# Performance work log

Hardware: AMD Instinct MI355X
Metric: run time of the kernel (lower is better)

## Reference

```python
import jax, jax.numpy as jnp
import numpy as np

B, S, E, KD = 4, 2048, 1024, 1024

def setup_inputs() -> dict:
    key = jax.random.key(0)
    k1, k2, k3, k4 = jax.random.split(key, 4)
    # nn.Linear weights are [out_features, in_features]
    x = jax.random.normal(k1, (B, S, E), dtype=jnp.float32)
    W_q = jax.random.normal(k2, (KD, E), dtype=jnp.float32) * (E ** -0.5)
    W_k = jax.random.normal(k3, (KD, E), dtype=jnp.float32) * (E ** -0.5)
    W_v = jax.random.normal(k4, (E, E), dtype=jnp.float32) * (E ** -0.5)
    return {"x": x, "W_q": W_q, "W_k": W_k, "W_v": W_v}

def reference(x, W_q, W_k, W_v):
    # Projections: y = x @ W.T  (torch Linear convention)
    Q = jnp.einsum('bse,ke->bsk', x, W_q)   # [B,S,KD]
    K = jnp.einsum('bse,ke->bsk', x, W_k)   # [B,S,KD]
    V = jnp.einsum('bse,fe->bsf', x, W_v)   # [B,S,E]
    key_dim = W_q.shape[0]
    scores = jnp.einsum('bqk,bsk->bqs', Q, K) / jnp.sqrt(jnp.asarray(key_dim, x.dtype))
    S_len = x.shape[1]
    causal = jnp.tril(jnp.ones((S_len, S_len), dtype=bool))  # [S,S]
    scores = jnp.where(causal, scores, -jnp.inf)
    weights = jax.nn.softmax(scores, axis=-1)                # [B,S,S]
    out = jnp.einsum('bqs,bsf->bqf', weights, V)             # [B,S,E]
    return out
```

## Files before the change

### kernel.cpp

```cpp
#include <hip/hip_runtime.h>

typedef _Float16 f16;
typedef _Float16 f16x8 __attribute__((ext_vector_type(8)));
typedef float    f32x4 __attribute__((ext_vector_type(4)));

__device__ __forceinline__ void gld_lds16(const void* g, void* l) {
    __builtin_amdgcn_global_load_lds((__attribute__((address_space(1))) void*)g,
                                     (__attribute__((address_space(3))) void*)l,
                                     16, 0, 0);
}

#define BARRIER() do { asm volatile("" ::: "memory"); \
                       __builtin_amdgcn_s_barrier();  \
                       asm volatile("" ::: "memory"); } while (0)

template<bool SB, bool SA, int VM>
__device__ __forceinline__ void tile256(
    f32x4 (&acc)[8][4],
    const f16* Ak0, const f16* Ak1, const f16* Bk0, const f16* Bk1,
    const f16* gBn, f16* lBn,
    const f16* gAn, f16* lAn,
    int lda, int ldb)
{
    f16x8 a0[8], a1[8], b0[4], b1[4];
    #pragma unroll
    for (int mf = 0; mf < 8; mf++) a0[mf] = *(const f16x8*)(Ak0 + mf * 1024);
    #pragma unroll
    for (int nf = 0; nf < 4; nf++) b0[nf] = *(const f16x8*)(Bk0 + nf * 1024);
    if (SB) {
        gld_lds16(gBn,                  lBn);
        gld_lds16(gBn + (long)64 * ldb, lBn + 4096);
    }
    BARRIER();
    __builtin_amdgcn_s_setprio(1);
    #pragma unroll
    for (int mf = 0; mf < 4; mf++)
        #pragma unroll
        for (int nf = 0; nf < 4; nf++)
            acc[mf][nf] = __builtin_amdgcn_mfma_f32_16x16x32_f16(
                a0[mf], b0[nf], acc[mf][nf], 0, 0, 0);
    __builtin_amdgcn_s_setprio(0);
    BARRIER();
    #pragma unroll
    for (int mf = 0; mf < 8; mf++) a1[mf] = *(const f16x8*)(Ak1 + mf * 1024);
    #pragma unroll
    for (int nf = 0; nf < 4; nf++) b1[nf] = *(const f16x8*)(Bk1 + nf * 1024);
    if (SB) {
        gld_lds16(gBn + (long)128 * ldb, lBn + 8192);
        gld_lds16(gBn + (long)192 * ldb, lBn + 12288);
    }
    BARRIER();
    __builtin_amdgcn_s_setprio(1);
    #pragma unroll
    for (int mf = 4; mf < 8; mf++)
        #pragma unroll
        for (int nf = 0; nf < 4; nf++)
            acc[mf][nf] = __builtin_amdgcn_mfma_f32_16x16x32_f16(
                a0[mf], b0[nf], acc[mf][nf], 0, 0, 0);
    __builtin_amdgcn_s_setprio(0);
    asm volatile("s_waitcnt lgkmcnt(0)" ::: "memory");
    BARRIER();
    if (SA) {
        gld_lds16(gAn,                  lAn);
        gld_lds16(gAn + (long)64 * lda, lAn + 4096);
    }
    BARRIER();
    __builtin_amdgcn_s_setprio(1);
    #pragma unroll
    for (int mf = 0; mf < 4; mf++)
        #pragma unroll
        for (int nf = 0; nf < 4; nf++)
            acc[mf][nf] = __builtin_amdgcn_mfma_f32_16x16x32_f16(
                a1[mf], b1[nf], acc[mf][nf], 0, 0, 0);
    __builtin_amdgcn_s_setprio(0);
    BARRIER();
    if (SA) {
        gld_lds16(gAn + (long)128 * lda, lAn + 8192);
        gld_lds16(gAn + (long)192 * lda, lAn + 12288);
    }
    BARRIER();
    __builtin_amdgcn_s_setprio(1);
    #pragma unroll
    for (int mf = 4; mf < 8; mf++)
        #pragma unroll
        for (int nf = 0; nf < 4; nf++)
            acc[mf][nf] = __builtin_amdgcn_mfma_f32_16x16x32_f16(
                a1[mf], b1[nf], acc[mf][nf], 0, 0, 0);
    __builtin_amdgcn_s_setprio(0);
    if (VM == 4)      asm volatile("s_waitcnt vmcnt(4)" ::: "memory");
    else if (VM == 0) asm volatile("s_waitcnt vmcnt(0)" ::: "memory");
    BARRIER();
}

__global__ void __launch_bounds__(512, 2)
gemm256_k1024(const f16* __restrict__ A, const f16* __restrict__ B,
              f16* __restrict__ C, int lda, int ldb, int ldc)
{
    const int i0 = blockIdx.y * 256;
    const int j0 = blockIdx.x * 256;

    __shared__ f16 L[2 * 32768] __attribute__((aligned(16)));

    const int tid  = threadIdx.x;
    const int lane = tid & 63;
    const int wave = tid >> 6;
    const int wm = wave >> 2, wn = wave & 3;
    const int row16 = lane & 15, quad = lane >> 4;
    const int swz = row16 & 7;

    const int c0 = (quad ^ swz) * 8;
    const int c1 = ((quad + 4) ^ swz) * 8;
    const f16* A0k0 = L + (wm * 128 + row16) * 64 + c0;
    const f16* A0k1 = L + (wm * 128 + row16) * 64 + c1;
    const f16* B0k0 = L + 16384 + (wn * 64 + row16) * 64 + c0;
    const f16* B0k1 = L + 16384 + (wn * 64 + row16) * 64 + c1;

    const int srow = tid >> 3;
    const int scol = ((tid & 7) ^ (srow & 7)) * 8;
    const f16* gA = A + (long)(i0 + srow) * lda + scol;
    const f16* gB = B + (long)(j0 + srow) * ldb + scol;
    f16* lA0 = L + tid * 8;
    f16* lB0 = L + 16384 + tid * 8;
    f16* lA1 = L + 32768 + tid * 8;
    f16* lB1 = L + 32768 + 16384 + tid * 8;

    gld_lds16(gA,                   lA0);
    gld_lds16(gA + (long)64 * lda,  lA0 + 4096);
    gld_lds16(gA + (long)128 * lda, lA0 + 8192);
    gld_lds16(gA + (long)192 * lda, lA0 + 12288);
    gld_lds16(gB,                   lB0);
    gld_lds16(gB + (long)64 * ldb,  lB0 + 4096);
    gld_lds16(gB + (long)128 * ldb, lB0 + 8192);
    gld_lds16(gB + (long)192 * ldb, lB0 + 12288);
    gld_lds16(gA + 64,                   lA1);
    gld_lds16(gA + 64 + (long)64 * lda,  lA1 + 4096);
    gld_lds16(gA + 64 + (long)128 * lda, lA1 + 8192);
    gld_lds16(gA + 64 + (long)192 * lda, lA1 + 12288);

    f32x4 acc[8][4] = {};

    asm volatile("s_waitcnt vmcnt(4)" ::: "memory");
    BARRIER();

    for (int t = 0; t < 14; t += 2) {
        tile256<true, true, 4>(acc, A0k0, A0k1, B0k0, B0k1,
                               gB + (t + 1) * 64, lB1,
                               gA + (t + 2) * 64, lA0, lda, ldb);
        tile256<true, true, 4>(acc, A0k0 + 32768, A0k1 + 32768,
                               B0k0 + 32768, B0k1 + 32768,
                               gB + (t + 2) * 64, lB0,
                               gA + (t + 3) * 64, lA1, lda, ldb);
    }
    tile256<true, false, 0>(acc, A0k0, A0k1, B0k0, B0k1,
                            gB + 15 * 64, lB1, nullptr, nullptr, lda, ldb);
    tile256<false, false, -1>(acc, A0k0 + 32768, A0k1 + 32768,
                              B0k0 + 32768, B0k1 + 32768,
                              nullptr, nullptr, nullptr, nullptr, lda, ldb);

    #pragma unroll
    for (int mf = 0; mf < 8; mf++) {
        const int r0 = i0 + wm * 128 + mf * 16 + quad * 4;
        #pragma unroll
        for (int nf = 0; nf < 4; nf++) {
            const int c = j0 + wn * 64 + nf * 16 + row16;
            #pragma unroll
            for (int r = 0; r < 4; r++)
                C[(long)(r0 + r) * ldc + c] = (f16)acc[mf][nf][r];
        }
    }
}

template<typename OutT, int MODE>
__global__ void __launch_bounds__(256)
gemm_bt(const f16* __restrict__ A, const f16* __restrict__ B, OutT* __restrict__ C,
        int lda, int ldb, int ldc, int K, float scale,
        long sA, long sB, long sC)
{
    const int bz = blockIdx.z;
    A += (long)bz * sA;
    B += (long)bz * sB;
    C += (long)bz * sC;

    int bx = blockIdx.x, by = blockIdx.y;
    if (MODE == 1) {
        const int t = bx;
        int y = 0;
        while ((y + 1) * (y + 2) <= t) y++;
        by = y;
        bx = t - y * (y + 1);
    }
    if (MODE == 2 && (blockIdx.z & 2)) by = (int)gridDim.y - 1 - by;

    const int i0 = by * 128;
    const int j0 = bx * 64;
    int Keff = K;
    if (MODE == 2) Keff = min(K, i0 + 128);

    __shared__ f16 As[128 * 64] __attribute__((aligned(16)));
    __shared__ f16 Bs[64 * 64]  __attribute__((aligned(16)));

    const int tid  = threadIdx.x;
    const int lane = tid & 63;
    const int wave = tid >> 6;
    const int row16 = lane & 15;
    const int quad  = lane >> 4;
    const int swz   = row16 & 7;
    const int wr = (wave >> 1) * 64;
    const int wc = (wave & 1) * 32;

    const int srow = tid >> 3;
    const int scol = ((tid & 7) ^ (srow & 7)) * 8;
    const f16* gA = A + (long)(i0 + srow) * lda + scol;
    const f16* gB = B + (long)(j0 + srow) * ldb + scol;
    f16* lA = As + tid * 8;
    f16* lB = Bs + tid * 8;

    f32x4 acc[4][2] = {};

    for (int k0 = 0; k0 < Keff; k0 += 64) {
        gld_lds16(gA + k0,                  lA);
        gld_lds16(gA + k0 + (long)32 * lda, lA + 32 * 64);
        gld_lds16(gA + k0 + (long)64 * lda, lA + 64 * 64);
        gld_lds16(gA + k0 + (long)96 * lda, lA + 96 * 64);
        gld_lds16(gB + k0,                  lB);
        gld_lds16(gB + k0 + (long)32 * ldb, lB + 32 * 64);
        __syncthreads();

        #pragma unroll
        for (int kk = 0; kk < 2; kk++) {
            f16x8 af[4], bf[2];
            #pragma unroll
            for (int t = 0; t < 4; t++)
                af[t] = *(const f16x8*)(As + (wr + t * 16 + row16) * 64
                                           + (((kk * 4 + quad) ^ swz) * 8));
            #pragma unroll
            for (int t = 0; t < 2; t++)
                bf[t] = *(const f16x8*)(Bs + (wc + t * 16 + row16) * 64
                                           + (((kk * 4 + quad) ^ swz) * 8));
            #pragma unroll
            for (int mt = 0; mt < 4; mt++)
                #pragma unroll
                for (int nt = 0; nt < 2; nt++)
                    acc[mt][nt] = __builtin_amdgcn_mfma_f32_16x16x32_f16(
                        af[mt], bf[nt], acc[mt][nt], 0, 0, 0);
        }
        __syncthreads();
    }

    #pragma unroll
    for (int mt = 0; mt < 4; mt++) {
        const int r0 = i0 + wr + mt * 16 + quad * 4;
        #pragma unroll
        for (int nt = 0; nt < 2; nt++) {
            const int c = j0 + wc + nt * 16 + row16;
            #pragma unroll
            for (int r = 0; r < 4; r++)
                C[(long)(r0 + r) * ldc + c] = (OutT)(acc[mt][nt][r] * scale);
        }
    }
}

__global__ void __launch_bounds__(256)
softmax_causal(f16* __restrict__ Sc)
{
    const int S = 2048;
    const long rowg = blockIdx.x;
    const long b = rowg >> 11;
    const int  i = (int)(rowg & 2047);
    f16* row = Sc + ((b * S + i) * (long)S);
    const int L = ((i >> 7) + 1) << 7;

    const int tid = threadIdx.x;
    const int c0  = tid * 8;
    const int lane = tid & 63, wave = tid >> 6;
    const bool act = c0 < L;

    float v[8];
    float m = -3.4e38f;
    if (act) {
        f16x8 in = *(const f16x8*)(row + c0);
        #pragma unroll
        for (int j = 0; j < 8; j++) {
            const bool ok = (c0 + j) <= i;
            v[j] = ok ? (float)in[j] : -3.4e38f;
            m = fmaxf(m, v[j]);
        }
    }
    #pragma unroll
    for (int off = 32; off > 0; off >>= 1)
        m = fmaxf(m, __shfl_down(m, off, 64));
    __shared__ float redm[4];
    if (lane == 0) redm[wave] = m;
    __syncthreads();
    const float m0 = fmaxf(fmaxf(redm[0], redm[1]), fmaxf(redm[2], redm[3]));

    float e[8];
    float s = 0.f;
    if (act) {
        #pragma unroll
        for (int j = 0; j < 8; j++) {
            const bool ok = (c0 + j) <= i;
            e[j] = ok ? __expf(v[j] - m0) : 0.f;
            s += e[j];
        }
    }
    #pragma unroll
    for (int off = 32; off > 0; off >>= 1)
        s += __shfl_down(s, off, 64);
    __shared__ float reds[4];
    if (lane == 0) reds[wave] = s;
    __syncthreads();
    const float inv = 1.f / (reds[0] + reds[1] + reds[2] + reds[3]);

    if (act) {
        f16x8 o;
        #pragma unroll
        for (int j = 0; j < 8; j++) o[j] = (f16)(e[j] * inv);
        *(f16x8*)(row + c0) = o;
    }
}

__global__ void __launch_bounds__(256)
convert_all(const float* __restrict__ x, const float* __restrict__ Wq,
            const float* __restrict__ Wk, const float* __restrict__ Wv,
            f16* __restrict__ xh, f16* __restrict__ wh)
{
    const long blk = blockIdx.x;
    const float* src;
    f16* dst;
    long base;
    if (blk < 4096)      { src = x;  dst = xh;                    base = blk * 2048; }
    else if (blk < 4608) { src = Wq; dst = wh;                    base = (blk - 4096) * 2048; }
    else if (blk < 5120) { src = Wk; dst = wh + 1024L * 1024;     base = (blk - 4608) * 2048; }
    else                 { src = Wv; dst = wh + 2L * 1024 * 1024; base = (blk - 5120) * 2048; }
    const long i = base + (long)threadIdx.x * 8;
    f32x4 a = *(const f32x4*)(src + i);
    f32x4 b = *(const f32x4*)(src + i + 4);
    f16x8 o;
    o[0] = (f16)a[0]; o[1] = (f16)a[1]; o[2] = (f16)a[2]; o[3] = (f16)a[3];
    o[4] = (f16)b[0]; o[5] = (f16)b[1]; o[6] = (f16)b[2]; o[7] = (f16)b[3];
    *(f16x8*)(dst + i) = o;
}

extern "C" void kernel_launch(void* const* d_in, const int* in_sizes, int n_in,
                              void* d_out, int out_size, void* d_ws, size_t ws_size,
                              hipStream_t stream)
{
    (void)in_sizes; (void)n_in; (void)out_size; (void)ws_size;
    const float* x  = (const float*)d_in[0];
    const float* Wq = (const float*)d_in[1];
    const float* Wk = (const float*)d_in[2];
    const float* Wv = (const float*)d_in[3];
    float* out = (float*)d_out;

    const long NX = 4L * 2048 * 1024;
    const long NW = 1024L * 1024;

    char* p = (char*)d_ws;
    f16* xh  = (f16*)p; p += NX * 2;
    f16* wh  = (f16*)p; p += 3 * NW * 2;
    f16* QKh = (f16*)p; p += 2 * NX * 2;
    f16* Vt  = (f16*)p; p += NX * 2;
    f16* Sc  = (f16*)p; p += 4L * 2048 * 2048 * 2;
    f16* wvh = wh + 2L * NW;

    convert_all<<<5632, 256, 0, stream>>>(x, Wq, Wk, Wv, xh, wh);

    gemm256_k1024<<<dim3(8, 32, 1), 512, 0, stream>>>(
        xh, wh, QKh, 1024, 1024, 2048);
    gemm_bt<f16, 0><<<dim3(128, 8, 1), 256, 0, stream>>>(
        wvh, xh, Vt, 1024, 1024, 8192, 1024, 1.f, 0, 0, 0);

    gemm_bt<f16, 1><<<dim3(272, 1, 4), 256, 0, stream>>>(
        QKh, QKh + 1024, Sc, 2048, 2048, 2048, 1024, 0.03125f,
        2048L * 2048, 2048L * 2048, 2048L * 2048);

    softmax_causal<<<4 * 2048, 256, 0, stream>>>(Sc);

    gemm_bt<float, 2><<<dim3(16, 16, 4), 256, 0, stream>>>(
        Sc, Vt, out, 2048, 8192, 1024, 2048, 1.f,
        2048L * 2048, 2048L, 2048L * 1024);
}
```

Measured before the change: 248.2 us.

## Restage 256x256 GEMM pipeline to load A and B together with finer waits

```diff
diff --git a/kernel.cpp b/kernel.cpp
--- a/kernel.cpp
+++ b/kernel.cpp
@@ -14,82 +14,94 @@
                        __builtin_amdgcn_s_barrier();  \
                        asm volatile("" ::: "memory"); } while (0)
 
-template<bool SB, bool SA, int VM>
+template<bool STG, int VM1, int VM4>
 __device__ __forceinline__ void tile256(
     f32x4 (&acc)[8][4],
     const f16* Ak0, const f16* Ak1, const f16* Bk0, const f16* Bk1,
-    const f16* gBn, f16* lBn,
-    const f16* gAn, f16* lAn,
+    const f16* gAn, const f16* gBn,
+    f16* lAn, f16* lBn,
     int lda, int ldb)
 {
-    f16x8 a0[8], a1[8], b0[4], b1[4];
-    #pragma unroll
-    for (int mf = 0; mf < 8; mf++) a0[mf] = *(const f16x8*)(Ak0 + mf * 1024);
-    #pragma unroll
-    for (int nf = 0; nf < 4; nf++) b0[nf] = *(const f16x8*)(Bk0 + nf * 1024);
-    if (SB) {
-        gld_lds16(gBn,                  lBn);
-        gld_lds16(gBn + (long)64 * ldb, lBn + 4096);
-    }
-    BARRIER();
-    __builtin_amdgcn_s_setprio(1);
-    #pragma unroll
-    for (int mf = 0; mf < 4; mf++)
-        #pragma unroll
-        for (int nf = 0; nf < 4; nf++)
-            acc[mf][nf] = __builtin_amdgcn_mfma_f32_16x16x32_f16(
-                a0[mf], b0[nf], acc[mf][nf], 0, 0, 0);
-    __builtin_amdgcn_s_setprio(0);
-    BARRIER();
-    #pragma unroll
-    for (int mf = 0; mf < 8; mf++) a1[mf] = *(const f16x8*)(Ak1 + mf * 1024);
-    #pragma unroll
-    for (int nf = 0; nf < 4; nf++) b1[nf] = *(const f16x8*)(Bk1 + nf * 1024);
-    if (SB) {
-        gld_lds16(gBn + (long)128 * ldb, lBn + 8192);
-        gld_lds16(gBn + (long)192 * ldb, lBn + 12288);
-    }
-    BARRIER();
-    __builtin_amdgcn_s_setprio(1);
-    #pragma unroll
-    for (int mf = 4; mf < 8; mf++)
-        #pragma unroll
-        for (int nf = 0; nf < 4; nf++)
-            acc[mf][nf] = __builtin_amdgcn_mfma_f32_16x16x32_f16(
-                a0[mf], b0[nf], acc[mf][nf], 0, 0, 0);
-    __builtin_amdgcn_s_setprio(0);
-    asm volatile("s_waitcnt lgkmcnt(0)" ::: "memory");
-    BARRIER();
-    if (SA) {
-        gld_lds16(gAn,                  lAn);
-        gld_lds16(gAn + (long)64 * lda, lAn + 4096);
-    }
-    BARRIER();
-    __builtin_amdgcn_s_setprio(1);
-    #pragma unroll
-    for (int mf = 0; mf < 4; mf++)
-        #pragma unroll
-        for (int nf = 0; nf < 4; nf++)
-            acc[mf][nf] = __builtin_amdgcn_mfma_f32_16x16x32_f16(
-                a1[mf], b1[nf], acc[mf][nf], 0, 0, 0);
-    __builtin_amdgcn_s_setprio(0);
-    BARRIER();
-    if (SA) {
-        gld_lds16(gAn + (long)128 * lda, lAn + 8192);
-        gld_lds16(gAn + (long)192 * lda, lAn + 12288);
-    }
-    BARRIER();
-    __builtin_amdgcn_s_setprio(1);
-    #pragma unroll
-    for (int mf = 4; mf < 8; mf++)
-        #pragma unroll
-        for (int nf = 0; nf < 4; nf++)
-            acc[mf][nf] = __builtin_amdgcn_mfma_f32_16x16x32_f16(
-                a1[mf], b1[nf], acc[mf][nf], 0, 0, 0);
-    __builtin_amdgcn_s_setprio(0);
-    if (VM == 4)      asm volatile("s_waitcnt vmcnt(4)" ::: "memory");
-    else if (VM == 0) asm volatile("s_waitcnt vmcnt(0)" ::: "memory");
-    BARRIER();
+    {
+        f16x8 a[4], b[4];
+        #pragma unroll
+        for (int mf = 0; mf < 4; mf++) a[mf] = *(const f16x8*)(Ak0 + mf * 1024);
+        #pragma unroll
+        for (int nf = 0; nf < 4; nf++) b[nf] = *(const f16x8*)(Bk0 + nf * 1024);
+        if (STG) {
+            gld_lds16(gBn,                  lBn);
+            gld_lds16(gBn + (long)64 * ldb, lBn + 4096);
+        }
+        BARRIER();
+        __builtin_amdgcn_s_setprio(1);
+        #pragma unroll
+        for (int mf = 0; mf < 4; mf++)
+            #pragma unroll
+            for (int nf = 0; nf < 4; nf++)
+                acc[mf][nf] = __builtin_amdgcn_mfma_f32_16x16x32_f16(
+                    a[mf], b[nf], acc[mf][nf], 0, 0, 0);
+        __builtin_amdgcn_s_setprio(0);
+        if (VM1 == 2)      asm volatile("s_waitcnt vmcnt(2)" ::: "memory");
+        else if (VM1 == 0) asm volatile("s_waitcnt vmcnt(0)" ::: "memory");
+        BARRIER();
+        f16x8 a2[4];
+        #pragma unroll
+        for (int mf = 0; mf < 4; mf++) a2[mf] = *(const f16x8*)(Ak0 + (mf + 4) * 1024);
+        if (STG) {
+            gld_lds16(gBn + (long)128 * ldb, lBn + 8192);
+            gld_lds16(gBn + (long)192 * ldb, lBn + 12288);
+        }
+        BARRIER();
+        __builtin_amdgcn_s_setprio(1);
+        #pragma unroll
+        for (int mf = 0; mf < 4; mf++)
+            #pragma unroll
+            for (int nf = 0; nf < 4; nf++)
+                acc[mf + 4][nf] = __builtin_amdgcn_mfma_f32_16x16x32_f16(
+                    a2[mf], b[nf], acc[mf + 4][nf], 0, 0, 0);
+        __builtin_amdgcn_s_setprio(0);
+        BARRIER();
+    }
+    {
+        f16x8 a[4], b[4];
+        #pragma unroll
+        for (int mf = 0; mf < 4; mf++) a[mf] = *(const f16x8*)(Ak1 + mf * 1024);
+        #pragma unroll
+        for (int nf = 0; nf < 4; nf++) b[nf] = *(const f16x8*)(Bk1 + nf * 1024);
+        if (STG) {
+            gld_lds16(gAn,                   lAn);
+            gld_lds16(gAn + (long)128 * lda, lAn + 8192);
+        }
+        BARRIER();
+        __builtin_amdgcn_s_setprio(1);
+        #pragma unroll
+        for (int mf = 0; mf < 4; mf++)
+            #pragma unroll
+            for (int nf = 0; nf < 4; nf++)
+                acc[mf][nf] = __builtin_amdgcn_mfma_f32_16x16x32_f16(
+                    a[mf], b[nf], acc[mf][nf], 0, 0, 0);
+        __builtin_amdgcn_s_setprio(0);
+        BARRIER();
+        f16x8 a2[4];
+        #pragma unroll
+        for (int mf = 0; mf < 4; mf++) a2[mf] = *(const f16x8*)(Ak1 + (mf + 4) * 1024);
+        if (STG) {
+            gld_lds16(gAn + (long)64 * lda,  lAn + 4096);
+            gld_lds16(gAn + (long)192 * lda, lAn + 12288);
+        }
+        BARRIER();
+        __builtin_amdgcn_s_setprio(1);
+        #pragma unroll
+        for (int mf = 0; mf < 4; mf++)
+            #pragma unroll
+            for (int nf = 0; nf < 4; nf++)
+                acc[mf + 4][nf] = __builtin_amdgcn_mfma_f32_16x16x32_f16(
+                    a2[mf], b[nf], acc[mf + 4][nf], 0, 0, 0);
+        __builtin_amdgcn_s_setprio(0);
+        if (VM4 == 2)      asm volatile("s_waitcnt vmcnt(2)" ::: "memory");
+        else if (VM4 == 0) asm volatile("s_waitcnt vmcnt(0)" ::: "memory");
+        BARRIER();
+    }
 }
 
 __global__ void __launch_bounds__(512, 2)
@@ -124,38 +136,34 @@
     f16* lA1 = L + 32768 + tid * 8;
     f16* lB1 = L + 32768 + 16384 + tid * 8;
 
-    gld_lds16(gA,                   lA0);
-    gld_lds16(gA + (long)64 * lda,  lA0 + 4096);
-    gld_lds16(gA + (long)128 * lda, lA0 + 8192);
-    gld_lds16(gA + (long)192 * lda, lA0 + 12288);
     gld_lds16(gB,                   lB0);
     gld_lds16(gB + (long)64 * ldb,  lB0 + 4096);
     gld_lds16(gB + (long)128 * ldb, lB0 + 8192);
     gld_lds16(gB + (long)192 * ldb, lB0 + 12288);
-    gld_lds16(gA + 64,                   lA1);
-    gld_lds16(gA + 64 + (long)64 * lda,  lA1 + 4096);
-    gld_lds16(gA + 64 + (long)128 * lda, lA1 + 8192);
-    gld_lds16(gA + 64 + (long)192 * lda, lA1 + 12288);
+    gld_lds16(gA,                   lA0);
+    gld_lds16(gA + (long)128 * lda, lA0 + 8192);
+    gld_lds16(gA + (long)64 * lda,  lA0 + 4096);
+    gld_lds16(gA + (long)192 * lda, lA0 + 12288);
 
     f32x4 acc[8][4] = {};
 
-    asm volatile("s_waitcnt vmcnt(4)" ::: "memory");
+    asm volatile("s_waitcnt vmcnt(2)" ::: "memory");
     BARRIER();
 
     for (int t = 0; t < 14; t += 2) {
-        tile256<true, true, 4>(acc, A0k0, A0k1, B0k0, B0k1,
-                               gB + (t + 1) * 64, lB1,
-                               gA + (t + 2) * 64, lA0, lda, ldb);
-        tile256<true, true, 4>(acc, A0k0 + 32768, A0k1 + 32768,
-                               B0k0 + 32768, B0k1 + 32768,
-                               gB + (t + 2) * 64, lB0,
-                               gA + (t + 3) * 64, lA1, lda, ldb);
-    }
-    tile256<true, false, 0>(acc, A0k0, A0k1, B0k0, B0k1,
-                            gB + 15 * 64, lB1, nullptr, nullptr, lda, ldb);
-    tile256<false, false, -1>(acc, A0k0 + 32768, A0k1 + 32768,
-                              B0k0 + 32768, B0k1 + 32768,
-                              nullptr, nullptr, nullptr, nullptr, lda, ldb);
+        tile256<true, 2, 2>(acc, A0k0, A0k1, B0k0, B0k1,
+                            gA + (t + 1) * 64, gB + (t + 1) * 64,
+                            lA1, lB1, lda, ldb);
+        tile256<true, 2, 2>(acc, A0k0 + 32768, A0k1 + 32768,
+                            B0k0 + 32768, B0k1 + 32768,
+                            gA + (t + 2) * 64, gB + (t + 2) * 64,
+                            lA0, lB0, lda, ldb);
+    }
+    tile256<true, 2, 2>(acc, A0k0, A0k1, B0k0, B0k1,
+                        gA + 15 * 64, gB + 15 * 64, lA1, lB1, lda, ldb);
+    tile256<false, 0, -1>(acc, A0k0 + 32768, A0k1 + 32768,
+                          B0k0 + 32768, B0k1 + 32768,
+                          nullptr, nullptr, nullptr, nullptr, lda, ldb);
 
     #pragma unroll
     for (int mf = 0; mf < 8; mf++) {
```

Measured after the change: 237.0 us. 1.05x faster.
